# Optimization experiments

Hardware: AMD Instinct MI355X
Metric: run time of the kernel (lower is better)

Reference implementation:

```python
import jax, jax.numpy as jnp
import numpy as np

N_NODES = 80000


def gcn_conv(x, src, dst, W, b, n_nodes):
    """PyG-style GCNConv: add self-loops, symmetric deg normalization,
    out = D^{-1/2} (A+I) D^{-1/2} (x @ W) + b."""
    h = x @ W  # [N, F_out] transform before gather (as PyG does)
    loop = jnp.arange(n_nodes, dtype=src.dtype)
    s = jnp.concatenate([src, loop])
    d = jnp.concatenate([dst, loop])
    deg = jax.ops.segment_sum(jnp.ones_like(s, dtype=h.dtype), d, num_segments=n_nodes)
    dinv = jnp.where(deg > 0, jax.lax.rsqrt(deg), 0.0)
    norm = dinv[s] * dinv[d]  # [E+N]
    msgs = h[s] * norm[:, None]  # gather + scale (memory-bound)
    out = jax.ops.segment_sum(msgs, d, num_segments=n_nodes)
    return out + b


def setup_inputs() -> dict:
    key = jax.random.key(0)
    ks = jax.random.split(key, 8)
    N, E, F = N_NODES, 640000, 128
    x = jax.random.normal(ks[0], (N, F), dtype=jnp.float32)
    edge_index = jax.random.randint(ks[1], (2, E), 0, N, dtype=jnp.int32)
    eps = jax.random.normal(ks[2], (N, F), dtype=jnp.float32)
    sc = 1.0 / np.sqrt(F)
    W1 = jax.random.normal(ks[3], (F, F), dtype=jnp.float32) * sc
    Wmu = jax.random.normal(ks[4], (F, F), dtype=jnp.float32) * sc
    Wlv = jax.random.normal(ks[5], (F, F), dtype=jnp.float32) * sc
    b1 = jnp.zeros((F,), jnp.float32)
    bmu = jnp.zeros((F,), jnp.float32)
    blv = jnp.zeros((F,), jnp.float32)
    return {"x": x, "edge_index": edge_index, "eps": eps,
            "W1": W1, "b1": b1, "Wmu": Wmu, "bmu": bmu, "Wlv": Wlv, "blv": blv}


def reference(x, edge_index, eps, W1, b1, Wmu, bmu, Wlv, blv):
    n = x.shape[0]
    src, dst = edge_index[0], edge_index[1]
    # encode
    h = jax.nn.relu(gcn_conv(x, src, dst, W1, b1, n))
    mu = gcn_conv(h, src, dst, Wmu, bmu, n)
    logvar = gcn_conv(h, src, dst, Wlv, blv, n)
    # reparameterize (training mode)
    z = eps * jnp.exp(0.5 * logvar) + mu
    # decode (reuses conv1, so out_channels == in_channels)
    recon = jax.nn.sigmoid(gcn_conv(z, src, dst, W1, b1, n))
    return recon, mu, logvar
```

## Files before the change

### kernel.cpp

```cpp
#include <hip/hip_runtime.h>
#include <hip/hip_bf16.h>

#define FDIM 128

typedef __attribute__((ext_vector_type(8))) short short8;
typedef __attribute__((ext_vector_type(4))) float f32x4;

__device__ inline float bflo(unsigned u) { return __uint_as_float(u << 16); }
__device__ inline float bfhi(unsigned u) { return __uint_as_float(u & 0xffff0000u); }
__device__ inline unsigned short f2bf(float f) {
    unsigned u = __float_as_uint(f);
    u += 0x7fffu + ((u >> 16) & 1u);
    return (unsigned short)(u >> 16);
}
__device__ inline unsigned pack2(float a, float b) {
    return (unsigned)f2bf(a) | ((unsigned)f2bf(b) << 16);
}

__global__ __launch_bounds__(256) void deg_kernel(const int* __restrict__ dst, int* __restrict__ cnt, int E) {
    int e = blockIdx.x * 256 + threadIdx.x;
    if (e < E) atomicAdd(&cnt[dst[e]], 1);
}

__global__ __launch_bounds__(256) void scan_partial(const int* __restrict__ cnt, int* __restrict__ bsum, int n) {
    __shared__ int sdata[256];
    int b = blockIdx.x, t = threadIdx.x;
    int base = b * 1024;
    int s = 0;
    for (int i = 0; i < 4; i++) {
        int idx = base + t * 4 + i;
        if (idx < n) s += cnt[idx];
    }
    sdata[t] = s;
    __syncthreads();
    for (int off = 128; off > 0; off >>= 1) {
        if (t < off) sdata[t] += sdata[t + off];
        __syncthreads();
    }
    if (t == 0) bsum[b] = sdata[0];
}

__global__ __launch_bounds__(256) void scan_sums(int* __restrict__ bsum, int nb) {
    __shared__ int sdata[256];
    int t = threadIdx.x;
    int v = (t < nb) ? bsum[t] : 0;
    sdata[t] = v;
    __syncthreads();
    for (int off = 1; off < 256; off <<= 1) {
        int u = (t >= off) ? sdata[t - off] : 0;
        __syncthreads();
        sdata[t] += u;
        __syncthreads();
    }
    if (t < nb) bsum[t] = sdata[t] - v;
}

__global__ __launch_bounds__(256) void scan_final(const int* __restrict__ cnt, const int* __restrict__ bsum,
                                                  int* __restrict__ rowptr, int n, int E) {
    __shared__ int sdata[256];
    int b = blockIdx.x, t = threadIdx.x;
    int base = b * 1024;
    int loc[4];
    int s = 0;
    for (int i = 0; i < 4; i++) {
        int idx = base + t * 4 + i;
        int v = (idx < n) ? cnt[idx] : 0;
        loc[i] = s;
        s += v;
    }
    sdata[t] = s;
    __syncthreads();
    for (int off = 1; off < 256; off <<= 1) {
        int v = (t >= off) ? sdata[t - off] : 0;
        __syncthreads();
        sdata[t] += v;
        __syncthreads();
    }
    int texc = sdata[t] - s;
    int boff = bsum[b];
    for (int i = 0; i < 4; i++) {
        int idx = base + t * 4 + i;
        if (idx < n) rowptr[idx] = boff + texc + loc[i];
    }
    if (b == 0 && t == 0) rowptr[n] = E;
}

__global__ __launch_bounds__(256) void deg_dinv(const int* __restrict__ cnt, float* __restrict__ dinv, int n) {
    int i = blockIdx.x * 256 + threadIdx.x;
    if (i < n) dinv[i] = rsqrtf((float)(cnt[i] + 1));
}

__global__ __launch_bounds__(256) void fill_kernel(const int* __restrict__ srcI, const int* __restrict__ dstI,
                                                   const int* __restrict__ rowptr, int* __restrict__ fill,
                                                   int* __restrict__ col, int E) {
    int e = blockIdx.x * 256 + threadIdx.x;
    if (e < E) {
        int d = dstI[e];
        int pos = rowptr[d] + atomicAdd(&fill[d], 1);
        col[pos] = srcI[e];
    }
}

template<bool BF16IN>
__global__ __launch_bounds__(256) void gemm_mfma(const void* __restrict__ Xv, const float* __restrict__ W,
                                                 const float* __restrict__ dinv, unsigned short* __restrict__ Y,
                                                 int n) {
    __shared__ unsigned short Wt[128][136];
    int t = threadIdx.x;
    #pragma unroll 4
    for (int i = 0; i < 64; i++) {
        int idx = i * 256 + t;
        int r = idx >> 7, c = idx & 127;
        Wt[c][r] = f2bf(W[idx]);
    }
    __syncthreads();

    int wave = t >> 6, lane = t & 63;
    int quad = lane >> 4, mrow = lane & 15;
    int row0 = blockIdx.x * 64 + wave * 16;
    int gr = row0 + mrow; if (gr >= n) gr = n - 1;

    f32x4 acc[8];
    #pragma unroll
    for (int i = 0; i < 8; i++) acc[i] = (f32x4){0.f, 0.f, 0.f, 0.f};

    #pragma unroll
    for (int kb = 0; kb < 4; kb++) {
        int k0 = kb * 32 + quad * 8;
        short8 a;
        if (BF16IN) {
            union { uint4 u4; short8 s8; } cv;
            cv.u4 = *(const uint4*)((const unsigned short*)Xv + (size_t)gr * FDIM + k0);
            a = cv.s8;
        } else {
            const float* xp = (const float*)Xv + (size_t)gr * FDIM + k0;
            float4 f0 = *(const float4*)xp;
            float4 f1 = *(const float4*)(xp + 4);
            union { unsigned u[4]; short8 s8; } cv;
            cv.u[0] = pack2(f0.x, f0.y); cv.u[1] = pack2(f0.z, f0.w);
            cv.u[2] = pack2(f1.x, f1.y); cv.u[3] = pack2(f1.z, f1.w);
            a = cv.s8;
        }
        #pragma unroll
        for (int tile = 0; tile < 8; tile++) {
            short8 b = *(const short8*)&Wt[tile * 16 + mrow][k0];
            acc[tile] = __builtin_amdgcn_mfma_f32_16x16x32_bf16(a, b, acc[tile], 0, 0, 0);
        }
    }

    #pragma unroll
    for (int r = 0; r < 4; r++) {
        int rowg = row0 + quad * 4 + r;
        if (rowg < n) {
            float dj = dinv[rowg];
            #pragma unroll
            for (int tile = 0; tile < 8; tile++)
                Y[(size_t)rowg * FDIM + tile * 16 + mrow] = f2bf(acc[tile][r] * dj);
        }
    }
}

template<int MODE>
__global__ __launch_bounds__(256) void agg_bf16(const uint4* __restrict__ T0, const int* __restrict__ rowptr,
                                                const int* __restrict__ col, const float* __restrict__ dinv,
                                                const float* __restrict__ bias, float* __restrict__ outF,
                                                unsigned short* __restrict__ outB, const float* __restrict__ eps,
                                                const float* __restrict__ mu, int n) {
    int t = threadIdx.x;
    int lane16 = t & 15;
    int node = blockIdx.x * 16 + (t >> 4);
    if (node >= n) return;

    size_t ridx = (size_t)node * 16 + lane16;
    float acc[8];
    {
        uint4 v = T0[ridx];
        acc[0] = bflo(v.x); acc[1] = bfhi(v.x); acc[2] = bflo(v.y); acc[3] = bfhi(v.y);
        acc[4] = bflo(v.z); acc[5] = bfhi(v.z); acc[6] = bflo(v.w); acc[7] = bfhi(v.w);
    }

    int rp0 = rowptr[node], rp1 = rowptr[node + 1];
    for (int eb = rp0; eb < rp1; eb += 16) {
        int e = eb + lane16;
        int myc = (e < rp1) ? col[e] : 0;
        int m = rp1 - eb; if (m > 16) m = 16;
        for (int i = 0; i < m; i++) {
            int s = __shfl(myc, i, 16);
            uint4 v = T0[(size_t)s * 16 + lane16];
            acc[0] += bflo(v.x); acc[1] += bfhi(v.x); acc[2] += bflo(v.y); acc[3] += bfhi(v.y);
            acc[4] += bflo(v.z); acc[5] += bfhi(v.z); acc[6] += bflo(v.w); acc[7] += bfhi(v.w);
        }
    }

    float dj = dinv[node];
    float4 b0 = *(const float4*)(bias + lane16 * 8);
    float4 b1 = *(const float4*)(bias + lane16 * 8 + 4);
    float r[8];
    r[0] = acc[0] * dj + b0.x; r[1] = acc[1] * dj + b0.y;
    r[2] = acc[2] * dj + b0.z; r[3] = acc[3] * dj + b0.w;
    r[4] = acc[4] * dj + b1.x; r[5] = acc[5] * dj + b1.y;
    r[6] = acc[6] * dj + b1.z; r[7] = acc[7] * dj + b1.w;

    size_t fo = (size_t)node * FDIM + lane16 * 8;
    if (MODE == 0) {
        uint4 o;
        o.x = pack2(fmaxf(r[0], 0.f), fmaxf(r[1], 0.f));
        o.y = pack2(fmaxf(r[2], 0.f), fmaxf(r[3], 0.f));
        o.z = pack2(fmaxf(r[4], 0.f), fmaxf(r[5], 0.f));
        o.w = pack2(fmaxf(r[6], 0.f), fmaxf(r[7], 0.f));
        ((uint4*)outB)[ridx] = o;
    } else if (MODE == 1) {
        *(float4*)(outF + fo)     = (float4){r[0], r[1], r[2], r[3]};
        *(float4*)(outF + fo + 4) = (float4){r[4], r[5], r[6], r[7]};
    } else if (MODE == 2) {
        *(float4*)(outF + fo)     = (float4){r[0], r[1], r[2], r[3]};
        *(float4*)(outF + fo + 4) = (float4){r[4], r[5], r[6], r[7]};
        float4 e0 = *(const float4*)(eps + fo), e1 = *(const float4*)(eps + fo + 4);
        float4 m0 = *(const float4*)(mu + fo),  m1 = *(const float4*)(mu + fo + 4);
        float z0 = e0.x * expf(0.5f * r[0]) + m0.x;
        float z1 = e0.y * expf(0.5f * r[1]) + m0.y;
        float z2 = e0.z * expf(0.5f * r[2]) + m0.z;
        float z3 = e0.w * expf(0.5f * r[3]) + m0.w;
        float z4 = e1.x * expf(0.5f * r[4]) + m1.x;
        float z5 = e1.y * expf(0.5f * r[5]) + m1.y;
        float z6 = e1.z * expf(0.5f * r[6]) + m1.z;
        float z7 = e1.w * expf(0.5f * r[7]) + m1.w;
        uint4 o;
        o.x = pack2(z0, z1); o.y = pack2(z2, z3); o.z = pack2(z4, z5); o.w = pack2(z6, z7);
        ((uint4*)outB)[ridx] = o;
    } else {
        *(float4*)(outF + fo) = (float4){1.f / (1.f + expf(-r[0])), 1.f / (1.f + expf(-r[1])),
                                         1.f / (1.f + expf(-r[2])), 1.f / (1.f + expf(-r[3]))};
        *(float4*)(outF + fo + 4) = (float4){1.f / (1.f + expf(-r[4])), 1.f / (1.f + expf(-r[5])),
                                             1.f / (1.f + expf(-r[6])), 1.f / (1.f + expf(-r[7]))};
    }
}

extern "C" void kernel_launch(void* const* d_in, const int* in_sizes, int n_in,
                              void* d_out, int out_size, void* d_ws, size_t ws_size,
                              hipStream_t stream) {
    const int F = FDIM;
    const int N = in_sizes[0] / F;
    const int E = in_sizes[1] / 2;

    const float* x   = (const float*)d_in[0];
    const int*   ei  = (const int*)d_in[1];
    const int*   srcI = ei;
    const int*   dstI = ei + E;
    const float* eps = (const float*)d_in[2];
    const float* W1  = (const float*)d_in[3];
    const float* b1  = (const float*)d_in[4];
    const float* Wmu = (const float*)d_in[5];
    const float* bmu = (const float*)d_in[6];
    const float* Wlv = (const float*)d_in[7];
    const float* blv = (const float*)d_in[8];

    float* recon = (float*)d_out;
    size_t NF = (size_t)N * F;
    float* muO = recon + NF;
    float* lvO = recon + 2 * NF;

    size_t off = 0;
    auto alloc = [&](size_t bytes) -> void* {
        void* p = (char*)d_ws + off;
        off += (bytes + 255) & ~(size_t)255;
        return p;
    };
    int*   cnt    = (int*)alloc((size_t)N * 4);
    int*   rowptr = (int*)alloc((size_t)(N + 1) * 4);
    int*   fillc  = (int*)alloc((size_t)N * 4);
    int*   bsum   = (int*)alloc(4096);
    int*   col    = (int*)alloc((size_t)E * 4);
    float* dinv   = (float*)alloc((size_t)N * 4);
    unsigned short* t0 = (unsigned short*)alloc(NF * 2);
    unsigned short* h  = (unsigned short*)alloc(NF * 2);
    unsigned short* z  = (unsigned short*)alloc(NF * 2);

    hipMemsetAsync(cnt, 0, (size_t)N * 4, stream);
    hipMemsetAsync(fillc, 0, (size_t)N * 4, stream);

    int eb = (E + 255) / 256;
    int NB = (N + 1023) / 1024;
    deg_kernel<<<eb, 256, 0, stream>>>(dstI, cnt, E);
    scan_partial<<<NB, 256, 0, stream>>>(cnt, bsum, N);
    scan_sums<<<1, 256, 0, stream>>>(bsum, NB);
    scan_final<<<NB, 256, 0, stream>>>(cnt, bsum, rowptr, N, E);
    deg_dinv<<<(N + 255) / 256, 256, 0, stream>>>(cnt, dinv, N);
    fill_kernel<<<eb, 256, 0, stream>>>(srcI, dstI, rowptr, fillc, col, E);

    int gb = (N + 63) / 64;
    int ab = (N + 15) / 16;

    gemm_mfma<false><<<gb, 256, 0, stream>>>(x, W1, dinv, t0, N);
    agg_bf16<0><<<ab, 256, 0, stream>>>((const uint4*)t0, rowptr, col, dinv, b1, nullptr, h, nullptr, nullptr, N);
    gemm_mfma<true><<<gb, 256, 0, stream>>>(h, Wmu, dinv, t0, N);
    agg_bf16<1><<<ab, 256, 0, stream>>>((const uint4*)t0, rowptr, col, dinv, bmu, muO, nullptr, nullptr, nullptr, N);
    gemm_mfma<true><<<gb, 256, 0, stream>>>(h, Wlv, dinv, t0, N);
    agg_bf16<2><<<ab, 256, 0, stream>>>((const uint4*)t0, rowptr, col, dinv, blv, lvO, z, eps, muO, N);
    gemm_mfma<true><<<gb, 256, 0, stream>>>(z, W1, dinv, t0, N);
    agg_bf16<3><<<ab, 256, 0, stream>>>((const uint4*)t0, rowptr, col, dinv, b1, recon, nullptr, nullptr, nullptr, N);
}
```

Measured before the change: 468.0 us.

## Reorder to aggregate-then-transform and share the mu/logvar aggregation

Uses the identity Â(XW) = (ÂX)W to run the sparse gather before the dense GEMM. Because mu and logvar share input h, one aggregation now feeds a dual GEMM that computes both, which removes one of the four gather passes. The epilogues (bias, relu, reparameterize, sigmoid) move into the GEMM kernels, and the gather loop is unrolled by four to keep more loads in flight. The cost is an extra conv_scale pass over x, and the GEMM outputs are now written with strided scalar stores instead of vectorized ones.

```diff
diff --git a/kernel.cpp b/kernel.cpp
--- a/kernel.cpp
+++ b/kernel.cpp
@@ -101,17 +101,84 @@
     }
 }
 
-template<bool BF16IN>
-__global__ __launch_bounds__(256) void gemm_mfma(const void* __restrict__ Xv, const float* __restrict__ W,
-                                                 const float* __restrict__ dinv, unsigned short* __restrict__ Y,
-                                                 int n) {
+__global__ __launch_bounds__(256) void conv_scale(const float* __restrict__ X, const float* __restrict__ dinv,
+                                                  uint4* __restrict__ Y, int nf8) {
+    int i = blockIdx.x * 256 + threadIdx.x;
+    if (i >= nf8) return;
+    int row = i >> 4;
+    float d = dinv[row];
+    const float4* X4 = (const float4*)X;
+    float4 f0 = X4[i * 2], f1 = X4[i * 2 + 1];
+    uint4 o;
+    o.x = pack2(f0.x * d, f0.y * d);
+    o.y = pack2(f0.z * d, f0.w * d);
+    o.z = pack2(f1.x * d, f1.y * d);
+    o.w = pack2(f1.z * d, f1.w * d);
+    Y[i] = o;
+}
+
+__global__ __launch_bounds__(256) void gather_agg(const uint4* __restrict__ T, const int* __restrict__ rowptr,
+                                                  const int* __restrict__ col, const float* __restrict__ dinv,
+                                                  uint4* __restrict__ G, int n) {
+    int t = threadIdx.x;
+    int lane16 = t & 15;
+    int node = blockIdx.x * 16 + (t >> 4);
+    if (node >= n) return;
+
+    size_t ridx = (size_t)node * 16 + lane16;
+    float acc[8];
+    {
+        uint4 v = T[ridx];
+        acc[0] = bflo(v.x); acc[1] = bfhi(v.x); acc[2] = bflo(v.y); acc[3] = bfhi(v.y);
+        acc[4] = bflo(v.z); acc[5] = bfhi(v.z); acc[6] = bflo(v.w); acc[7] = bfhi(v.w);
+    }
+    auto add8 = [&](uint4 v) {
+        acc[0] += bflo(v.x); acc[1] += bfhi(v.x); acc[2] += bflo(v.y); acc[3] += bfhi(v.y);
+        acc[4] += bflo(v.z); acc[5] += bfhi(v.z); acc[6] += bflo(v.w); acc[7] += bfhi(v.w);
+    };
+
+    int rp0 = rowptr[node], rp1 = rowptr[node + 1];
+    for (int eb = rp0; eb < rp1; eb += 16) {
+        int e = eb + lane16;
+        int myc = (e < rp1) ? col[e] : 0;
+        int m = rp1 - eb; if (m > 16) m = 16;
+        int i = 0;
+        for (; i + 4 <= m; i += 4) {
+            int s0 = __shfl(myc, i, 16);
+            int s1 = __shfl(myc, i + 1, 16);
+            int s2 = __shfl(myc, i + 2, 16);
+            int s3 = __shfl(myc, i + 3, 16);
+            uint4 v0 = T[(size_t)s0 * 16 + lane16];
+            uint4 v1 = T[(size_t)s1 * 16 + lane16];
+            uint4 v2 = T[(size_t)s2 * 16 + lane16];
+            uint4 v3 = T[(size_t)s3 * 16 + lane16];
+            add8(v0); add8(v1); add8(v2); add8(v3);
+        }
+        for (; i < m; i++) {
+            int s = __shfl(myc, i, 16);
+            add8(T[(size_t)s * 16 + lane16]);
+        }
+    }
+
+    float dj = dinv[node];
+    uint4 o;
+    o.x = pack2(acc[0] * dj, acc[1] * dj);
+    o.y = pack2(acc[2] * dj, acc[3] * dj);
+    o.z = pack2(acc[4] * dj, acc[5] * dj);
+    o.w = pack2(acc[6] * dj, acc[7] * dj);
+    G[ridx] = o;
+}
+
+template<int MODE>
+__global__ __launch_bounds__(256) void gemm_epi(const unsigned short* __restrict__ Gm, const float* __restrict__ W,
+                                                const float* __restrict__ bias, const float* __restrict__ dinv,
+                                                void* __restrict__ out, int n) {
     __shared__ unsigned short Wt[128][136];
     int t = threadIdx.x;
     #pragma unroll 4
     for (int i = 0; i < 64; i++) {
         int idx = i * 256 + t;
-        int r = idx >> 7, c = idx & 127;
-        Wt[c][r] = f2bf(W[idx]);
+        Wt[idx & 127][idx >> 7] = f2bf(W[idx]);
     }
     __syncthreads();
 
@@ -127,20 +194,9 @@
     #pragma unroll
     for (int kb = 0; kb < 4; kb++) {
         int k0 = kb * 32 + quad * 8;
-        short8 a;
-        if (BF16IN) {
-            union { uint4 u4; short8 s8; } cv;
-            cv.u4 = *(const uint4*)((const unsigned short*)Xv + (size_t)gr * FDIM + k0);
-            a = cv.s8;
-        } else {
-            const float* xp = (const float*)Xv + (size_t)gr * FDIM + k0;
-            float4 f0 = *(const float4*)xp;
-            float4 f1 = *(const float4*)(xp + 4);
-            union { unsigned u[4]; short8 s8; } cv;
-            cv.u[0] = pack2(f0.x, f0.y); cv.u[1] = pack2(f0.z, f0.w);
-            cv.u[2] = pack2(f1.x, f1.y); cv.u[3] = pack2(f1.z, f1.w);
-            a = cv.s8;
-        }
+        union { uint4 u4; short8 s8; } cv;
+        cv.u4 = *(const uint4*)(Gm + (size_t)gr * FDIM + k0);
+        short8 a = cv.s8;
         #pragma unroll
         for (int tile = 0; tile < 8; tile++) {
             short8 b = *(const short8*)&Wt[tile * 16 + mrow][k0];
@@ -151,88 +207,85 @@
     #pragma unroll
     for (int r = 0; r < 4; r++) {
         int rowg = row0 + quad * 4 + r;
-        if (rowg < n) {
+        if (rowg >= n) continue;
+        if (MODE == 0) {
             float dj = dinv[rowg];
+            unsigned short* Y = (unsigned short*)out;
             #pragma unroll
-            for (int tile = 0; tile < 8; tile++)
-                Y[(size_t)rowg * FDIM + tile * 16 + mrow] = f2bf(acc[tile][r] * dj);
-        }
-    }
-}
-
-template<int MODE>
-__global__ __launch_bounds__(256) void agg_bf16(const uint4* __restrict__ T0, const int* __restrict__ rowptr,
-                                                const int* __restrict__ col, const float* __restrict__ dinv,
-                                                const float* __restrict__ bias, float* __restrict__ outF,
-                                                unsigned short* __restrict__ outB, const float* __restrict__ eps,
-                                                const float* __restrict__ mu, int n) {
+            for (int tile = 0; tile < 8; tile++) {
+                int c = tile * 16 + mrow;
+                float v = fmaxf(acc[tile][r] + bias[c], 0.f) * dj;
+                Y[(size_t)rowg * FDIM + c] = f2bf(v);
+            }
+        } else {
+            float* Y = (float*)out;
+            #pragma unroll
+            for (int tile = 0; tile < 8; tile++) {
+                int c = tile * 16 + mrow;
+                float v = acc[tile][r] + bias[c];
+                Y[(size_t)rowg * FDIM + c] = 1.f / (1.f + expf(-v));
+            }
+        }
+    }
+}
+
+__global__ __launch_bounds__(256) void gemm_dual(const unsigned short* __restrict__ Gm,
+                                                 const float* __restrict__ Wmu, const float* __restrict__ Wlv,
+                                                 const float* __restrict__ bmu, const float* __restrict__ blv,
+                                                 const float* __restrict__ eps, const float* __restrict__ dinv,
+                                                 float* __restrict__ muO, float* __restrict__ lvO,
+                                                 unsigned short* __restrict__ zt, int n) {
+    __shared__ unsigned short Wa[128][136];
+    __shared__ unsigned short Wb[128][136];
     int t = threadIdx.x;
-    int lane16 = t & 15;
-    int node = blockIdx.x * 16 + (t >> 4);
-    if (node >= n) return;
-
-    size_t ridx = (size_t)node * 16 + lane16;
-    float acc[8];
-    {
-        uint4 v = T0[ridx];
-        acc[0] = bflo(v.x); acc[1] = bfhi(v.x); acc[2] = bflo(v.y); acc[3] = bfhi(v.y);
-        acc[4] = bflo(v.z); acc[5] = bfhi(v.z); acc[6] = bflo(v.w); acc[7] = bfhi(v.w);
-    }
-
-    int rp0 = rowptr[node], rp1 = rowptr[node + 1];
-    for (int eb = rp0; eb < rp1; eb += 16) {
-        int e = eb + lane16;
-        int myc = (e < rp1) ? col[e] : 0;
-        int m = rp1 - eb; if (m > 16) m = 16;
-        for (int i = 0; i < m; i++) {
-            int s = __shfl(myc, i, 16);
-            uint4 v = T0[(size_t)s * 16 + lane16];
-            acc[0] += bflo(v.x); acc[1] += bfhi(v.x); acc[2] += bflo(v.y); acc[3] += bfhi(v.y);
-            acc[4] += bflo(v.z); acc[5] += bfhi(v.z); acc[6] += bflo(v.w); acc[7] += bfhi(v.w);
-        }
-    }
-
-    float dj = dinv[node];
-    float4 b0 = *(const float4*)(bias + lane16 * 8);
-    float4 b1 = *(const float4*)(bias + lane16 * 8 + 4);
-    float r[8];
-    r[0] = acc[0] * dj + b0.x; r[1] = acc[1] * dj + b0.y;
-    r[2] = acc[2] * dj + b0.z; r[3] = acc[3] * dj + b0.w;
-    r[4] = acc[4] * dj + b1.x; r[5] = acc[5] * dj + b1.y;
-    r[6] = acc[6] * dj + b1.z; r[7] = acc[7] * dj + b1.w;
-
-    size_t fo = (size_t)node * FDIM + lane16 * 8;
-    if (MODE == 0) {
-        uint4 o;
-        o.x = pack2(fmaxf(r[0], 0.f), fmaxf(r[1], 0.f));
-        o.y = pack2(fmaxf(r[2], 0.f), fmaxf(r[3], 0.f));
-        o.z = pack2(fmaxf(r[4], 0.f), fmaxf(r[5], 0.f));
-        o.w = pack2(fmaxf(r[6], 0.f), fmaxf(r[7], 0.f));
-        ((uint4*)outB)[ridx] = o;
-    } else if (MODE == 1) {
-        *(float4*)(outF + fo)     = (float4){r[0], r[1], r[2], r[3]};
-        *(float4*)(outF + fo + 4) = (float4){r[4], r[5], r[6], r[7]};
-    } else if (MODE == 2) {
-        *(float4*)(outF + fo)     = (float4){r[0], r[1], r[2], r[3]};
-        *(float4*)(outF + fo + 4) = (float4){r[4], r[5], r[6], r[7]};
-        float4 e0 = *(const float4*)(eps + fo), e1 = *(const float4*)(eps + fo + 4);
-        float4 m0 = *(const float4*)(mu + fo),  m1 = *(const float4*)(mu + fo + 4);
-        float z0 = e0.x * expf(0.5f * r[0]) + m0.x;
-        float z1 = e0.y * expf(0.5f * r[1]) + m0.y;
-        float z2 = e0.z * expf(0.5f * r[2]) + m0.z;
-        float z3 = e0.w * expf(0.5f * r[3]) + m0.w;
-        float z4 = e1.x * expf(0.5f * r[4]) + m1.x;
-        float z5 = e1.y * expf(0.5f * r[5]) + m1.y;
-        float z6 = e1.z * expf(0.5f * r[6]) + m1.z;
-        float z7 = e1.w * expf(0.5f * r[7]) + m1.w;
-        uint4 o;
-        o.x = pack2(z0, z1); o.y = pack2(z2, z3); o.z = pack2(z4, z5); o.w = pack2(z6, z7);
-        ((uint4*)outB)[ridx] = o;
-    } else {
-        *(float4*)(outF + fo) = (float4){1.f / (1.f + expf(-r[0])), 1.f / (1.f + expf(-r[1])),
-                                         1.f / (1.f + expf(-r[2])), 1.f / (1.f + expf(-r[3]))};
-        *(float4*)(outF + fo + 4) = (float4){1.f / (1.f + expf(-r[4])), 1.f / (1.f + expf(-r[5])),
-                                             1.f / (1.f + expf(-r[6])), 1.f / (1.f + expf(-r[7]))};
+    #pragma unroll 4
+    for (int i = 0; i < 64; i++) {
+        int idx = i * 256 + t;
+        Wa[idx & 127][idx >> 7] = f2bf(Wmu[idx]);
+        Wb[idx & 127][idx >> 7] = f2bf(Wlv[idx]);
+    }
+    __syncthreads();
+
+    int wave = t >> 6, lane = t & 63;
+    int quad = lane >> 4, mrow = lane & 15;
+    int row0 = blockIdx.x * 64 + wave * 16;
+    int gr = row0 + mrow; if (gr >= n) gr = n - 1;
+
+    f32x4 am[8], al[8];
+    #pragma unroll
+    for (int i = 0; i < 8; i++) { am[i] = (f32x4){0.f,0.f,0.f,0.f}; al[i] = (f32x4){0.f,0.f,0.f,0.f}; }
+
+    #pragma unroll
+    for (int kb = 0; kb < 4; kb++) {
+        int k0 = kb * 32 + quad * 8;
+        union { uint4 u4; short8 s8; } cv;
+        cv.u4 = *(const uint4*)(Gm + (size_t)gr * FDIM + k0);
+        short8 a = cv.s8;
+        #pragma unroll
+        for (int tile = 0; tile < 8; tile++) {
+            short8 b0 = *(const short8*)&Wa[tile * 16 + mrow][k0];
+            am[tile] = __builtin_amdgcn_mfma_f32_16x16x32_bf16(a, b0, am[tile], 0, 0, 0);
+            short8 b1 = *(const short8*)&Wb[tile * 16 + mrow][k0];
+            al[tile] = __builtin_amdgcn_mfma_f32_16x16x32_bf16(a, b1, al[tile], 0, 0, 0);
+        }
+    }
+
+    #pragma unroll
+    for (int r = 0; r < 4; r++) {
+        int rowg = row0 + quad * 4 + r;
+        if (rowg >= n) continue;
+        float dj = dinv[rowg];
+        #pragma unroll
+        for (int tile = 0; tile < 8; tile++) {
+            int c = tile * 16 + mrow;
+            size_t o = (size_t)rowg * FDIM + c;
+            float m = am[tile][r] + bmu[c];
+            float l = al[tile][r] + blv[c];
+            muO[o] = m;
+            lvO[o] = l;
+            float z = eps[o] * expf(0.5f * l) + m;
+            zt[o] = f2bf(z * dj);
+        }
     }
 }
 
@@ -272,9 +325,8 @@
     int*   bsum   = (int*)alloc(4096);
     int*   col    = (int*)alloc((size_t)E * 4);
     float* dinv   = (float*)alloc((size_t)N * 4);
-    unsigned short* t0 = (unsigned short*)alloc(NF * 2);
-    unsigned short* h  = (unsigned short*)alloc(NF * 2);
-    unsigned short* z  = (unsigned short*)alloc(NF * 2);
+    unsigned short* bufA = (unsigned short*)alloc(NF * 2);
+    unsigned short* bufB = (unsigned short*)alloc(NF * 2);
 
     hipMemsetAsync(cnt, 0, (size_t)N * 4, stream);
     hipMemsetAsync(fillc, 0, (size_t)N * 4, stream);
@@ -288,15 +340,16 @@
     deg_dinv<<<(N + 255) / 256, 256, 0, stream>>>(cnt, dinv, N);
     fill_kernel<<<eb, 256, 0, stream>>>(srcI, dstI, rowptr, fillc, col, E);
 
+    int nf8 = (int)(NF / 8);
+    int cb = (nf8 + 255) / 256;
+    int ab = (N + 15) / 16;
     int gb = (N + 63) / 64;
-    int ab = (N + 15) / 16;
-
-    gemm_mfma<false><<<gb, 256, 0, stream>>>(x, W1, dinv, t0, N);
-    agg_bf16<0><<<ab, 256, 0, stream>>>((const uint4*)t0, rowptr, col, dinv, b1, nullptr, h, nullptr, nullptr, N);
-    gemm_mfma<true><<<gb, 256, 0, stream>>>(h, Wmu, dinv, t0, N);
-    agg_bf16<1><<<ab, 256, 0, stream>>>((const uint4*)t0, rowptr, col, dinv, bmu, muO, nullptr, nullptr, nullptr, N);
-    gemm_mfma<true><<<gb, 256, 0, stream>>>(h, Wlv, dinv, t0, N);
-    agg_bf16<2><<<ab, 256, 0, stream>>>((const uint4*)t0, rowptr, col, dinv, blv, lvO, z, eps, muO, N);
-    gemm_mfma<true><<<gb, 256, 0, stream>>>(z, W1, dinv, t0, N);
-    agg_bf16<3><<<ab, 256, 0, stream>>>((const uint4*)t0, rowptr, col, dinv, b1, recon, nullptr, nullptr, nullptr, N);
-}
+
+    conv_scale<<<cb, 256, 0, stream>>>(x, dinv, (uint4*)bufA, nf8);
+    gather_agg<<<ab, 256, 0, stream>>>((const uint4*)bufA, rowptr, col, dinv, (uint4*)bufB, N);
+    gemm_epi<0><<<gb, 256, 0, stream>>>(bufB, W1, b1, dinv, bufA, N);
+    gather_agg<<<ab, 256, 0, stream>>>((const uint4*)bufA, rowptr, col, dinv, (uint4*)bufB, N);
+    gemm_dual<<<gb, 256, 0, stream>>>(bufB, Wmu, Wlv, bmu, blv, eps, dinv, muO, lvO, bufA, N);
+    gather_agg<<<ab, 256, 0, stream>>>((const uint4*)bufA, rowptr, col, dinv, (uint4*)bufB, N);
+    gemm_epi<1><<<gb, 256, 0, stream>>>(bufB, W1, b1, nullptr, recon, N);
+}
```

New measurement: 425.1 us. 9.1% less time.
